# Performance work log

Hardware: AMD Instinct MI355X
Metric: run time of the kernel (lower is better)

Reference implementation:

```python
import jax, jax.numpy as jnp
import numpy as np

N = 4096      # num nodes == input_dim
HID = 1024    # VAE hidden
LAT = 512     # VAE latent
NH = 4        # GAT heads
NHID = 64     # per-head out features
ALPHA = 0.2   # leaky-relu negative slope
NEG_INF = -9e15


def setup_inputs() -> dict:
    key = jax.random.key(0)
    ks = iter(jax.random.split(key, 32))
    def lin(shape):
        return jax.random.normal(next(ks), shape, jnp.float32) / np.float32(np.sqrt(shape[-1]))
    inp = {
        "x": jax.random.uniform(next(ks), (N,), jnp.float32),
        "eps": jax.random.normal(next(ks), (LAT,), jnp.float32),
        "adj": jax.random.uniform(next(ks), (N, N), jnp.float32) < 0.01,  # ~40 nbrs/node
        "enc_w1": lin((HID, N)), "enc_b1": jnp.zeros((HID,), jnp.float32),
        "enc_w2": lin((HID, HID)), "enc_b2": jnp.zeros((HID,), jnp.float32),
        "enc_w3": lin((LAT, HID)), "enc_b3": jnp.zeros((LAT,), jnp.float32),
        "enc_w4": lin((LAT, HID)), "enc_b4": jnp.zeros((LAT,), jnp.float32),
        "dec_w1": lin((HID, LAT)), "dec_b1": jnp.zeros((HID,), jnp.float32),
        "dec_w2": lin((HID, HID)), "dec_b2": jnp.zeros((HID,), jnp.float32),
        "dec_w3": lin((N, HID)), "dec_b3": jnp.zeros((N,), jnp.float32),
        "gat_W": lin((NH, 1, NHID)),
        "gat_a": lin((NH, 2 * NHID, 1)),
        "out_W": lin((NH * NHID, 1)),
        "out_a": lin((2, 1)),
    }
    return inp


def _linear(h, w, b):
    return h @ w.T + b


def reference(x, eps, adj, enc_w1, enc_b1, enc_w2, enc_b2, enc_w3, enc_b3,
              enc_w4, enc_b4, dec_w1, dec_b1, dec_w2, dec_b2, dec_w3, dec_b3,
              gat_W, gat_a, out_W, out_a):
    # ---- VAE encoder ----
    h = jax.nn.relu(_linear(x, enc_w1, enc_b1))
    h = jax.nn.relu(_linear(h, enc_w2, enc_b2))
    mu = _linear(h, enc_w3, enc_b3)
    logvar = _linear(h, enc_w4, enc_b4)
    # ---- reparameterize ----
    z = mu + eps * jnp.exp(0.5 * logvar)
    # ---- VAE decoder ----
    h = jax.nn.relu(_linear(z, dec_w1, dec_b1))
    h = jax.nn.relu(_linear(h, dec_w2, dec_b2))
    x_hat = jax.nn.sigmoid(_linear(h, dec_w3, dec_b3))          # [N]

    # ---- GAT (eval mode: dropout = identity) ----
    def gat_layer(xin, W, a):
        Wh = xin @ W                                             # [N, F]
        f = W.shape[1]
        e = jax.nn.leaky_relu(Wh @ a[:f] + (Wh @ a[f:]).T, ALPHA)  # [N, N]
        e = jnp.where(adj, e, NEG_INF)
        att = jax.nn.softmax(e, axis=1)
        return att @ Wh                                          # [N, F]

    xf = x_hat[:, None]                                          # [N, 1]
    heads = jax.vmap(lambda W, a: gat_layer(xf, W, a))(gat_W, gat_a)  # [NH, N, NHID]
    hcat = jnp.transpose(heads, (1, 0, 2)).reshape(N, NH * NHID)      # concat dim=1
    y_hat = jax.nn.elu(gat_layer(hcat, out_W, out_a))            # [N, 1]

    return (x_hat, y_hat, mu, logvar)
```

## Files before the change

### kernel.cpp

```cpp
#include <hip/hip_runtime.h>
#include <cstdint>
#include <cstddef>


typedef unsigned long long u64;

#define ACT_NONE 0
#define ACT_RELU 1
#define ACT_SIG  2

__device__ __forceinline__ float d4(float4 a, float4 b) {
  return a.x * b.x + a.y * b.y + a.z * b.z + a.w * b.w;
}
__device__ __forceinline__ float waveRed(float v) {
  for (int o = 32; o; o >>= 1) v += __shfl_down(v, o);
  return v;
}

__device__ __forceinline__ void convRow(const uint4* aw, u64* bm, int r, int lane) {
  const uint4* rp = aw + (size_t)r * 1024u;
#pragma unroll
  for (int it = 0; it < 16; ++it) {
    const uint4 v = rp[it * 64 + lane];
    const u64 m0 = __ballot(v.x != 0u);
    const u64 m1 = __ballot(v.y != 0u);
    const u64 m2 = __ballot(v.z != 0u);
    const u64 m3 = __ballot(v.w != 0u);
    if (lane < 4) {
      const u64 mv = lane == 0 ? m0 : lane == 1 ? m1 : lane == 2 ? m2 : m3;
      bm[(size_t)r * 64 + it * 4 + lane] = mv;
    }
  }
}

struct MegaP {
  const void* adj;
  u64* bm;
  const float *w1, *x, *b1;
  float* h1;
  const float *gw, *ga, *ow, *oa;
  float* consts;
};

__global__ __launch_bounds__(256) void mega_kernel(MegaP p) {
  const int tid = threadIdx.x, w = tid >> 6, lane = tid & 63;
  const int blk = blockIdx.x;
  if (blk < 1024) {
    convRow((const uint4*)p.adj, p.bm, blk * 4 + w, lane);
    return;
  }
  if (blk < 2048) {
    const int r = blk - 1024;
    const float4* row = (const float4*)(p.w1 + (size_t)r * 4096u);
    const float4* x4 = (const float4*)p.x;
    float acc = 0.f;
#pragma unroll
    for (int k = 0; k < 4; ++k) {
      const int idx = tid + 256 * k;
      acc += d4(row[idx], x4[idx]);
    }
    acc = waveRed(acc);
    __shared__ float lds[4];
    if (lane == 0) lds[w] = acc;
    __syncthreads();
    if (tid == 0) {
      const float v = lds[0] + lds[1] + lds[2] + lds[3] + p.b1[r];
      p.h1[r] = v > 0.f ? v : 0.f;
    }
    return;
  }
  const int h = w, k = lane;
  const float wv = p.gw[h * 64 + k];
  float p1 = wv * p.ga[h * 128 + k];
  float p2 = wv * p.ga[h * 128 + 64 + k];
  float p3 = wv * p.ow[h * 64 + k];
  for (int off = 32; off; off >>= 1) {
    p1 += __shfl_down(p1, off);
    p2 += __shfl_down(p2, off);
    p3 += __shfl_down(p3, off);
  }
  if (k == 0) { p.consts[h] = p1; p.consts[4 + h] = p2; p.consts[8 + h] = p3; }
  if (tid == 0) { p.consts[12] = p.oa[0]; p.consts[13] = p.oa[1]; }
}

template<int ACT>
__global__ __launch_bounds__(256) void mv_kernel(const float* __restrict__ W,
    const float* __restrict__ x, const float* __restrict__ b,
    float* __restrict__ y, int C) {
  const int r = blockIdx.x;
  const float* row = W + (size_t)r * (size_t)C;
  float acc = 0.f;
  for (int c = threadIdx.x * 4; c < C; c += 256 * 4) {
    const float4 w4 = *reinterpret_cast<const float4*>(row + c);
    const float4 x4 = *reinterpret_cast<const float4*>(x + c);
    acc += d4(w4, x4);
  }
  acc = waveRed(acc);
  __shared__ float lds[4];
  if ((threadIdx.x & 63) == 0) lds[threadIdx.x >> 6] = acc;
  __syncthreads();
  if (threadIdx.x == 0) {
    float v = lds[0] + lds[1] + lds[2] + lds[3] + b[r];
    if (ACT == ACT_RELU) v = v > 0.f ? v : 0.f;
    if (ACT == ACT_SIG)  v = 1.f / (1.f + expf(-v));
    y[r] = v;
  }
}

__global__ __launch_bounds__(256) void mulv_kernel(const float* __restrict__ w3,
    const float* __restrict__ b3, const float* __restrict__ w4,
    const float* __restrict__ b4, const float* __restrict__ h2,
    float* __restrict__ mu, float* __restrict__ logvar) {
  const int r = blockIdx.x;
  const bool is_mu = r < 512;
  const int rr = is_mu ? r : r - 512;
  const float* row = (is_mu ? w3 : w4) + (size_t)rr * 1024u;
  const int c = threadIdx.x * 4;
  float acc = d4(*reinterpret_cast<const float4*>(row + c),
                 *reinterpret_cast<const float4*>(h2 + c));
  acc = waveRed(acc);
  __shared__ float lds[4];
  if ((threadIdx.x & 63) == 0) lds[threadIdx.x >> 6] = acc;
  __syncthreads();
  if (threadIdx.x == 0) {
    const float v = lds[0] + lds[1] + lds[2] + lds[3] + (is_mu ? b3[rr] : b4[rr]);
    (is_mu ? mu : logvar)[rr] = v;
  }
}

__global__ __launch_bounds__(256) void dec1_kernel(const float* __restrict__ W,
    const float* __restrict__ mu, const float* __restrict__ logvar,
    const float* __restrict__ eps, const float* __restrict__ b,
    float* __restrict__ y) {
  __shared__ float zsh[512];
  for (int k = threadIdx.x; k < 512; k += 256)
    zsh[k] = mu[k] + eps[k] * expf(0.5f * logvar[k]);
  __syncthreads();
  const int r = blockIdx.x;
  const float* row = W + (size_t)r * 512u;
  const int c = threadIdx.x * 2;
  const float2 w2 = *reinterpret_cast<const float2*>(row + c);
  float acc = w2.x * zsh[c] + w2.y * zsh[c + 1];
  acc = waveRed(acc);
  __shared__ float lds[4];
  if ((threadIdx.x & 63) == 0) lds[threadIdx.x >> 6] = acc;
  __syncthreads();
  if (threadIdx.x == 0) {
    float v = lds[0] + lds[1] + lds[2] + lds[3] + b[r];
    y[r] = v > 0.f ? v : 0.f;
  }
}

__global__ __launch_bounds__(256) void gat_heads_bm(const u64* __restrict__ bm,
    const float* __restrict__ xh, const float* __restrict__ consts,
    float* __restrict__ wh2) {
  const int lane = threadIdx.x & 63;
  const int i = blockIdx.x * 4 + (threadIdx.x >> 6);
  const float xi = xh[i];
  const float A0 = consts[0] * xi, A1 = consts[1] * xi,
              A2 = consts[2] * xi, A3 = consts[3] * xi;
  const float c20 = consts[4], c21 = consts[5], c22 = consts[6], c23 = consts[7];
  float s0 = 0, s1 = 0, s2 = 0, s3 = 0, t0 = 0, t1 = 0, t2 = 0, t3 = 0;
  u64 m = bm[(size_t)i * 64 + lane];
  const int qbase = ((lane >> 2) << 8) | (lane & 3);
  while (m) {
    const int bp = __builtin_ctzll(m);
    m &= m - 1;
    const float xj = xh[qbase + (bp << 2)];
    float e0 = A0 + c20 * xj, e1 = A1 + c21 * xj, e2 = A2 + c22 * xj, e3 = A3 + c23 * xj;
    e0 = fmaxf(e0, 0.2f * e0); e1 = fmaxf(e1, 0.2f * e1);
    e2 = fmaxf(e2, 0.2f * e2); e3 = fmaxf(e3, 0.2f * e3);
    const float w0 = expf(e0), w1 = expf(e1), w2 = expf(e2), w3 = expf(e3);
    s0 += w0; s1 += w1; s2 += w2; s3 += w3;
    t0 += w0 * xj; t1 += w1 * xj; t2 += w2 * xj; t3 += w3 * xj;
  }
  for (int o = 1; o < 64; o <<= 1) {
    s0 += __shfl_xor(s0, o); s1 += __shfl_xor(s1, o);
    s2 += __shfl_xor(s2, o); s3 += __shfl_xor(s3, o);
    t0 += __shfl_xor(t0, o); t1 += __shfl_xor(t1, o);
    t2 += __shfl_xor(t2, o); t3 += __shfl_xor(t3, o);
  }
  float r0, r1, r2, r3;
  if (s0 != 0.f) { r0 = t0 / s0; r1 = t1 / s1; r2 = t2 / s2; r3 = t3 / s3; }
  else {
    float a = 0.f;
    for (int k = lane; k < 4096; k += 64) a += xh[k];
    for (int o = 1; o < 64; o <<= 1) a += __shfl_xor(a, o);
    r0 = r1 = r2 = r3 = a * (1.f / 4096.f);
  }
  if (lane == 0)
    wh2[i] = consts[8] * r0 + consts[9] * r1 + consts[10] * r2 + consts[11] * r3;
}

__global__ __launch_bounds__(256) void gat_out_bm(const u64* __restrict__ bm,
    const float* __restrict__ wh2, const float* __restrict__ consts,
    float* __restrict__ yhat) {
  const int lane = threadIdx.x & 63;
  const int i = blockIdx.x * 4 + (threadIdx.x >> 6);
  const float Ai = consts[12] * wh2[i];
  const float oa1 = consts[13];
  float s = 0.f, t = 0.f;
  u64 m = bm[(size_t)i * 64 + lane];
  const int qbase = ((lane >> 2) << 8) | (lane & 3);
  while (m) {
    const int bp = __builtin_ctzll(m);
    m &= m - 1;
    const float wj = wh2[qbase + (bp << 2)];
    float e = Ai + oa1 * wj;
    e = fmaxf(e, 0.2f * e);
    const float ww = expf(e);
    s += ww; t += ww * wj;
  }
  for (int o = 1; o < 64; o <<= 1) {
    s += __shfl_xor(s, o);
    t += __shfl_xor(t, o);
  }
  float v;
  if (s != 0.f) v = t / s;
  else {
    float a = 0.f;
    for (int k = lane; k < 4096; k += 64) a += wh2[k];
    for (int o = 1; o < 64; o <<= 1) a += __shfl_xor(a, o);
    v = a * (1.f / 4096.f);
  }
  if (lane == 0) yhat[i] = v > 0.f ? v : expm1f(v);
}

extern "C" void kernel_launch(void* const* d_in, const int* in_sizes, int n_in,
                              void* d_out, int out_size, void* d_ws, size_t ws_size,
                              hipStream_t stream) {
  const float* x      = (const float*)d_in[0];
  const float* eps    = (const float*)d_in[1];
  const void*  adj    = d_in[2];
  const float* enc_w1 = (const float*)d_in[3];
  const float* enc_b1 = (const float*)d_in[4];
  const float* enc_w2 = (const float*)d_in[5];
  const float* enc_b2 = (const float*)d_in[6];
  const float* enc_w3 = (const float*)d_in[7];
  const float* enc_b3 = (const float*)d_in[8];
  const float* enc_w4 = (const float*)d_in[9];
  const float* enc_b4 = (const float*)d_in[10];
  const float* dec_w1 = (const float*)d_in[11];
  const float* dec_b1 = (const float*)d_in[12];
  const float* dec_w2 = (const float*)d_in[13];
  const float* dec_b2 = (const float*)d_in[14];
  const float* dec_w3 = (const float*)d_in[15];
  const float* dec_b3 = (const float*)d_in[16];
  const float* gat_W  = (const float*)d_in[17];
  const float* gat_a  = (const float*)d_in[18];
  const float* out_W  = (const float*)d_in[19];
  const float* out_a  = (const float*)d_in[20];

  float* out    = (float*)d_out;
  float* xhat   = out;
  float* yhat   = out + 4096;
  float* mu     = out + 8192;
  float* logvar = out + 8704;

  const size_t BM_BYTES = (size_t)4096 * 64 * sizeof(u64);
  u64*   bm     = (u64*)d_ws;
  float* F      = (float*)((char*)d_ws + BM_BYTES);
  float* h1     = F;
  float* h2     = F + 1024;
  float* h3     = F + 2048;
  float* h4     = F + 3072;
  float* wh2    = F + 4096;
  float* consts = F + 8208;

  MegaP mp;
  mp.adj = adj; mp.bm = bm;
  mp.w1 = enc_w1; mp.x = x; mp.b1 = enc_b1; mp.h1 = h1;
  mp.gw = gat_W; mp.ga = gat_a; mp.ow = out_W; mp.oa = out_a;
  mp.consts = consts;
  mega_kernel<<<2049, 256, 0, stream>>>(mp);

  mv_kernel<ACT_RELU><<<1024, 256, 0, stream>>>(enc_w2, h1, enc_b2, h2, 1024);
  mulv_kernel<<<1024, 256, 0, stream>>>(enc_w3, enc_b3, enc_w4, enc_b4, h2, mu, logvar);
  dec1_kernel<<<1024, 256, 0, stream>>>(dec_w1, mu, logvar, eps, dec_b1, h3);
  mv_kernel<ACT_RELU><<<1024, 256, 0, stream>>>(dec_w2, h3, dec_b2, h4, 1024);
  mv_kernel<ACT_SIG ><<<4096, 256, 0, stream>>>(dec_w3, h4, dec_b3, xhat, 1024);

  gat_heads_bm<<<1024, 256, 0, stream>>>(bm, xhat, consts, wh2);
  gat_out_bm<<<1024, 256, 0, stream>>>(bm, wh2, consts, yhat);
}
```

Before: 44.30 us.

## Spread adjacency bitmask conversion across the VAE matvec kernels

```diff
diff --git a/kernel.cpp b/kernel.cpp
--- a/kernel.cpp
+++ b/kernel.cpp
@@ -5,7 +5,6 @@
 
 typedef unsigned long long u64;
 
-#define ACT_NONE 0
 #define ACT_RELU 1
 #define ACT_SIG  2
 
@@ -33,6 +32,14 @@
   }
 }
 
+__device__ __forceinline__ bool convFirst(int CB, int convBase, const void* adj,
+                                          u64* bm) {
+  if ((int)blockIdx.x >= CB) return false;
+  const int row = convBase + blockIdx.x * 4 + (threadIdx.x >> 6);
+  convRow((const uint4*)adj, bm, row, threadIdx.x & 63);
+  return true;
+}
+
 struct MegaP {
   const void* adj;
   u64* bm;
@@ -45,12 +52,12 @@
 __global__ __launch_bounds__(256) void mega_kernel(MegaP p) {
   const int tid = threadIdx.x, w = tid >> 6, lane = tid & 63;
   const int blk = blockIdx.x;
-  if (blk < 1024) {
+  if (blk < 448) {
     convRow((const uint4*)p.adj, p.bm, blk * 4 + w, lane);
     return;
   }
-  if (blk < 2048) {
-    const int r = blk - 1024;
+  if (blk < 1472) {
+    const int r = blk - 448;
     const float4* row = (const float4*)(p.w1 + (size_t)r * 4096u);
     const float4* x4 = (const float4*)p.x;
     float acc = 0.f;
@@ -84,10 +91,12 @@
 }
 
 template<int ACT>
-__global__ __launch_bounds__(256) void mv_kernel(const float* __restrict__ W,
+__global__ __launch_bounds__(256) void mv_conv_kernel(const float* __restrict__ W,
     const float* __restrict__ x, const float* __restrict__ b,
-    float* __restrict__ y, int C) {
-  const int r = blockIdx.x;
+    float* __restrict__ y, int C, int CB, int convBase,
+    const void* __restrict__ adj, u64* __restrict__ bm) {
+  if (convFirst(CB, convBase, adj, bm)) return;
+  const int r = blockIdx.x - CB;
   const float* row = W + (size_t)r * (size_t)C;
   float acc = 0.f;
   for (int c = threadIdx.x * 4; c < C; c += 256 * 4) {
@@ -107,11 +116,13 @@
   }
 }
 
-__global__ __launch_bounds__(256) void mulv_kernel(const float* __restrict__ w3,
+__global__ __launch_bounds__(256) void mulv_conv_kernel(const float* __restrict__ w3,
     const float* __restrict__ b3, const float* __restrict__ w4,
     const float* __restrict__ b4, const float* __restrict__ h2,
-    float* __restrict__ mu, float* __restrict__ logvar) {
-  const int r = blockIdx.x;
+    float* __restrict__ mu, float* __restrict__ logvar, int CB, int convBase,
+    const void* __restrict__ adj, u64* __restrict__ bm) {
+  if (convFirst(CB, convBase, adj, bm)) return;
+  const int r = blockIdx.x - CB;
   const bool is_mu = r < 512;
   const int rr = is_mu ? r : r - 512;
   const float* row = (is_mu ? w3 : w4) + (size_t)rr * 1024u;
@@ -128,15 +139,17 @@
   }
 }
 
-__global__ __launch_bounds__(256) void dec1_kernel(const float* __restrict__ W,
+__global__ __launch_bounds__(256) void dec1_conv_kernel(const float* __restrict__ W,
     const float* __restrict__ mu, const float* __restrict__ logvar,
     const float* __restrict__ eps, const float* __restrict__ b,
-    float* __restrict__ y) {
+    float* __restrict__ y, int CB, int convBase,
+    const void* __restrict__ adj, u64* __restrict__ bm) {
+  if (convFirst(CB, convBase, adj, bm)) return;
   __shared__ float zsh[512];
   for (int k = threadIdx.x; k < 512; k += 256)
     zsh[k] = mu[k] + eps[k] * expf(0.5f * logvar[k]);
   __syncthreads();
-  const int r = blockIdx.x;
+  const int r = blockIdx.x - CB;
   const float* row = W + (size_t)r * 512u;
   const int c = threadIdx.x * 2;
   const float2 w2 = *reinterpret_cast<const float2*>(row + c);
@@ -272,13 +285,18 @@
   mp.w1 = enc_w1; mp.x = x; mp.b1 = enc_b1; mp.h1 = h1;
   mp.gw = gat_W; mp.ga = gat_a; mp.ow = out_W; mp.oa = out_a;
   mp.consts = consts;
-  mega_kernel<<<2049, 256, 0, stream>>>(mp);
-
-  mv_kernel<ACT_RELU><<<1024, 256, 0, stream>>>(enc_w2, h1, enc_b2, h2, 1024);
-  mulv_kernel<<<1024, 256, 0, stream>>>(enc_w3, enc_b3, enc_w4, enc_b4, h2, mu, logvar);
-  dec1_kernel<<<1024, 256, 0, stream>>>(dec_w1, mu, logvar, eps, dec_b1, h3);
-  mv_kernel<ACT_RELU><<<1024, 256, 0, stream>>>(dec_w2, h3, dec_b2, h4, 1024);
-  mv_kernel<ACT_SIG ><<<4096, 256, 0, stream>>>(dec_w3, h4, dec_b3, xhat, 1024);
+  mega_kernel<<<1473, 256, 0, stream>>>(mp);
+
+  mv_conv_kernel<ACT_RELU><<<96 + 1024, 256, 0, stream>>>(
+      enc_w2, h1, enc_b2, h2, 1024, 96, 1792, adj, bm);
+  mulv_conv_kernel<<<96 + 1024, 256, 0, stream>>>(
+      enc_w3, enc_b3, enc_w4, enc_b4, h2, mu, logvar, 96, 2176, adj, bm);
+  dec1_conv_kernel<<<96 + 1024, 256, 0, stream>>>(
+      dec_w1, mu, logvar, eps, dec_b1, h3, 96, 2560, adj, bm);
+  mv_conv_kernel<ACT_RELU><<<96 + 1024, 256, 0, stream>>>(
+      dec_w2, h3, dec_b2, h4, 1024, 96, 2944, adj, bm);
+  mv_conv_kernel<ACT_SIG><<<192 + 4096, 256, 0, stream>>>(
+      dec_w3, h4, dec_b3, xhat, 1024, 192, 3328, adj, bm);
 
   gat_heads_bm<<<1024, 256, 0, stream>>>(bm, xhat, consts, wh2);
   gat_out_bm<<<1024, 256, 0, stream>>>(bm, wh2, consts, yhat);
```

Result: slower. 60.23 us (+36.0%).

## Replace adjacency bitmask with per-row compact edge lists for GAT

Applied to the files above, without the earlier changes.

```diff
diff --git a/kernel.cpp b/kernel.cpp
--- a/kernel.cpp
+++ b/kernel.cpp
@@ -5,7 +5,6 @@
 
 typedef unsigned long long u64;
 
-#define ACT_NONE 0
 #define ACT_RELU 1
 #define ACT_SIG  2
 
@@ -17,25 +16,38 @@
   return v;
 }
 
-__device__ __forceinline__ void convRow(const uint4* aw, u64* bm, int r, int lane) {
+__device__ __forceinline__ void csrRow(const uint4* aw, unsigned short* edges,
+                                       unsigned* cnt, int r, int lane) {
   const uint4* rp = aw + (size_t)r * 1024u;
+  unsigned short* er = edges + (size_t)r * 1024u;
+  const u64 pm = (~0ull) >> (63 - lane);
+  const u64 pmb = pm >> 1;
+  unsigned total = 0;
 #pragma unroll
   for (int it = 0; it < 16; ++it) {
     const uint4 v = rp[it * 64 + lane];
-    const u64 m0 = __ballot(v.x != 0u);
-    const u64 m1 = __ballot(v.y != 0u);
-    const u64 m2 = __ballot(v.z != 0u);
-    const u64 m3 = __ballot(v.w != 0u);
-    if (lane < 4) {
-      const u64 mv = lane == 0 ? m0 : lane == 1 ? m1 : lane == 2 ? m2 : m3;
-      bm[(size_t)r * 64 + it * 4 + lane] = mv;
-    }
-  }
+    const int colb = it * 256 + 4 * lane;
+    u64 m;
+    m = __ballot(v.x != 0u);
+    if (v.x) er[min(total + (unsigned)__popcll(m & pmb), 1023u)] = (unsigned short)colb;
+    total += (unsigned)__popcll(m);
+    m = __ballot(v.y != 0u);
+    if (v.y) er[min(total + (unsigned)__popcll(m & pmb), 1023u)] = (unsigned short)(colb + 1);
+    total += (unsigned)__popcll(m);
+    m = __ballot(v.z != 0u);
+    if (v.z) er[min(total + (unsigned)__popcll(m & pmb), 1023u)] = (unsigned short)(colb + 2);
+    total += (unsigned)__popcll(m);
+    m = __ballot(v.w != 0u);
+    if (v.w) er[min(total + (unsigned)__popcll(m & pmb), 1023u)] = (unsigned short)(colb + 3);
+    total += (unsigned)__popcll(m);
+  }
+  if (lane == 0) cnt[r] = min(total, 1024u);
 }
 
 struct MegaP {
   const void* adj;
-  u64* bm;
+  unsigned short* edges;
+  unsigned* cnt;
   const float *w1, *x, *b1;
   float* h1;
   const float *gw, *ga, *ow, *oa;
@@ -46,7 +58,7 @@
   const int tid = threadIdx.x, w = tid >> 6, lane = tid & 63;
   const int blk = blockIdx.x;
   if (blk < 1024) {
-    convRow((const uint4*)p.adj, p.bm, blk * 4 + w, lane);
+    csrRow((const uint4*)p.adj, p.edges, p.cnt, blk * 4 + w, lane);
     return;
   }
   if (blk < 2048) {
@@ -151,22 +163,21 @@
   }
 }
 
-__global__ __launch_bounds__(256) void gat_heads_bm(const u64* __restrict__ bm,
+__global__ __launch_bounds__(256) void gat_heads_csr(
+    const unsigned short* __restrict__ edges, const unsigned* __restrict__ cnt,
     const float* __restrict__ xh, const float* __restrict__ consts,
     float* __restrict__ wh2) {
   const int lane = threadIdx.x & 63;
   const int i = blockIdx.x * 4 + (threadIdx.x >> 6);
+  const unsigned n = cnt[i];
   const float xi = xh[i];
   const float A0 = consts[0] * xi, A1 = consts[1] * xi,
               A2 = consts[2] * xi, A3 = consts[3] * xi;
   const float c20 = consts[4], c21 = consts[5], c22 = consts[6], c23 = consts[7];
   float s0 = 0, s1 = 0, s2 = 0, s3 = 0, t0 = 0, t1 = 0, t2 = 0, t3 = 0;
-  u64 m = bm[(size_t)i * 64 + lane];
-  const int qbase = ((lane >> 2) << 8) | (lane & 3);
-  while (m) {
-    const int bp = __builtin_ctzll(m);
-    m &= m - 1;
-    const float xj = xh[qbase + (bp << 2)];
+  const unsigned short* er = edges + (size_t)i * 1024u;
+  for (unsigned j = lane; j < n; j += 64) {
+    const float xj = xh[er[j]];
     float e0 = A0 + c20 * xj, e1 = A1 + c21 * xj, e2 = A2 + c22 * xj, e3 = A3 + c23 * xj;
     e0 = fmaxf(e0, 0.2f * e0); e1 = fmaxf(e1, 0.2f * e1);
     e2 = fmaxf(e2, 0.2f * e2); e3 = fmaxf(e3, 0.2f * e3);
@@ -181,7 +192,7 @@
     t2 += __shfl_xor(t2, o); t3 += __shfl_xor(t3, o);
   }
   float r0, r1, r2, r3;
-  if (s0 != 0.f) { r0 = t0 / s0; r1 = t1 / s1; r2 = t2 / s2; r3 = t3 / s3; }
+  if (n != 0) { r0 = t0 / s0; r1 = t1 / s1; r2 = t2 / s2; r3 = t3 / s3; }
   else {
     float a = 0.f;
     for (int k = lane; k < 4096; k += 64) a += xh[k];
@@ -192,20 +203,19 @@
     wh2[i] = consts[8] * r0 + consts[9] * r1 + consts[10] * r2 + consts[11] * r3;
 }
 
-__global__ __launch_bounds__(256) void gat_out_bm(const u64* __restrict__ bm,
+__global__ __launch_bounds__(256) void gat_out_csr(
+    const unsigned short* __restrict__ edges, const unsigned* __restrict__ cnt,
     const float* __restrict__ wh2, const float* __restrict__ consts,
     float* __restrict__ yhat) {
   const int lane = threadIdx.x & 63;
   const int i = blockIdx.x * 4 + (threadIdx.x >> 6);
+  const unsigned n = cnt[i];
   const float Ai = consts[12] * wh2[i];
   const float oa1 = consts[13];
   float s = 0.f, t = 0.f;
-  u64 m = bm[(size_t)i * 64 + lane];
-  const int qbase = ((lane >> 2) << 8) | (lane & 3);
-  while (m) {
-    const int bp = __builtin_ctzll(m);
-    m &= m - 1;
-    const float wj = wh2[qbase + (bp << 2)];
+  const unsigned short* er = edges + (size_t)i * 1024u;
+  for (unsigned j = lane; j < n; j += 64) {
+    const float wj = wh2[er[j]];
     float e = Ai + oa1 * wj;
     e = fmaxf(e, 0.2f * e);
     const float ww = expf(e);
@@ -216,7 +226,7 @@
     t += __shfl_xor(t, o);
   }
   float v;
-  if (s != 0.f) v = t / s;
+  if (n != 0) v = t / s;
   else {
     float a = 0.f;
     for (int k = lane; k < 4096; k += 64) a += wh2[k];
@@ -257,9 +267,9 @@
   float* mu     = out + 8192;
   float* logvar = out + 8704;
 
-  const size_t BM_BYTES = (size_t)4096 * 64 * sizeof(u64);
-  u64*   bm     = (u64*)d_ws;
-  float* F      = (float*)((char*)d_ws + BM_BYTES);
+  unsigned short* edges = (unsigned short*)d_ws;
+  unsigned* cnt = (unsigned*)((char*)d_ws + (size_t)4096 * 1024 * 2);
+  float* F      = (float*)((char*)cnt + 4096 * sizeof(unsigned));
   float* h1     = F;
   float* h2     = F + 1024;
   float* h3     = F + 2048;
@@ -268,7 +278,7 @@
   float* consts = F + 8208;
 
   MegaP mp;
-  mp.adj = adj; mp.bm = bm;
+  mp.adj = adj; mp.edges = edges; mp.cnt = cnt;
   mp.w1 = enc_w1; mp.x = x; mp.b1 = enc_b1; mp.h1 = h1;
   mp.gw = gat_W; mp.ga = gat_a; mp.ow = out_W; mp.oa = out_a;
   mp.consts = consts;
@@ -280,6 +290,6 @@
   mv_kernel<ACT_RELU><<<1024, 256, 0, stream>>>(dec_w2, h3, dec_b2, h4, 1024);
   mv_kernel<ACT_SIG ><<<4096, 256, 0, stream>>>(dec_w3, h4, dec_b3, xhat, 1024);
 
-  gat_heads_bm<<<1024, 256, 0, stream>>>(bm, xhat, consts, wh2);
-  gat_out_bm<<<1024, 256, 0, stream>>>(bm, wh2, consts, yhat);
-}
+  gat_heads_csr<<<1024, 256, 0, stream>>>(edges, cnt, xhat, consts, wh2);
+  gat_out_csr<<<1024, 256, 0, stream>>>(edges, cnt, wh2, consts, yhat);
+}
```

New measurement: 43.03 us. -2.9%, faster.
